# Optimization experiments

Measured on AMD Instinct MI355X. Metric: run time of the kernel, lower is better.

## Reference

```python
import jax, jax.numpy as jnp
import numpy as np

# loss weights / thresholds (match module defaults)
L_RC, L_HU, L_EDGE, L_TEX = 2.0, 1.5, 1.0, 0.8
L_HF, L_SYN, L_IC, L_MID, L_LF = 1.5, 1.0, 0.8, 0.8, 0.6
MIN_BODY, ART_FACTOR, FLAT_TH = 4096, 2.0, 0.03

SOBEL_X = jnp.array([[-1., 0., 1.], [-2., 0., 2.], [-1., 0., 1.]], jnp.float32)
SOBEL_Y = jnp.array([[-1., -2., -1.], [0., 0., 0.], [1., 2., 1.]], jnp.float32)
LAP = jnp.array([[0., 1., 0.], [1., -4., 1.], [0., 1., 0.]], jnp.float32)

def _conv2d(x, k):
    # x: (B,1,H,W), k: (kh,kw), 'same' padding single-channel conv
    kh, kw = k.shape
    return jax.lax.conv_general_dilated(
        x, k[None, None].astype(x.dtype), (1, 1),
        [(kh // 2, kh // 2), (kw // 2, kw // 2)],
        dimension_numbers=('NCHW', 'OIHW', 'NCHW'))

def _gauss_kernel(sigma):
    k = int(6 * sigma + 1)
    if k % 2 == 0:
        k += 1
    c = jnp.arange(k, dtype=jnp.float32) - k // 2
    g = jnp.exp(-0.5 * (c / sigma) ** 2)
    g = g / g.sum()
    return g[:, None] * g[None, :]

def _masked_mean(x, mask):
    cnt = jnp.sum(mask)
    return jnp.sum(jnp.where(mask, x, 0.0)) / jnp.maximum(cnt, 1)

def _masked_l1(a, b, mask):
    cnt = jnp.sum(mask)
    return jnp.sum(jnp.where(mask, jnp.abs(a - b), 0.0)) / jnp.maximum(cnt, 1)

def _masked_quantile(x, mask, q):
    # torch.quantile(x[mask], q) with linear interpolation
    v = jnp.sort(jnp.where(mask, x, jnp.inf).ravel())
    n = jnp.maximum(jnp.sum(mask), 1)
    pos = q * (n - 1).astype(x.dtype)
    lo = jnp.clip(jnp.floor(pos).astype(jnp.int32), 0, v.size - 1)
    hi = jnp.clip(jnp.ceil(pos).astype(jnp.int32), 0, v.size - 1)
    frac = pos - lo.astype(x.dtype)
    return v[lo] * (1.0 - frac) + v[hi] * frac

def setup_inputs() -> dict:
    key = jax.random.key(0)
    ks = jax.random.split(key, 7)
    B, H, W = 16, 768, 768
    return {
        'y_pred': jax.random.uniform(ks[0], (B, 1, 1, H, W), jnp.float32),
        'noise_pred': jax.random.normal(ks[1], (B, 1, 1, H, W), jnp.float32),
        'x_i': jax.random.uniform(ks[2], (B, 1, H, W), jnp.float32),
        'x_ip1': jax.random.uniform(ks[3], (B, 1, H, W), jnp.float32),
        'x_mid': jax.random.uniform(ks[4], (B, 1, H, W), jnp.float32),
        'W': jax.random.uniform(ks[5], (B, 1, H, W), jnp.float32),
        'noise_synthetic': jax.random.normal(ks[6], (B, 1, H, W), jnp.float32),
    }

def reference(y_pred, noise_pred, x_i, x_ip1, x_mid, W, noise_synthetic):
    yp = y_pred[:, :, 0]          # (B,1,H,W)
    npred = noise_pred[:, :, 0]

    # reconstruction
    loss_rc = jnp.mean(jnp.abs(yp * W - x_i * W))

    # HU consistency on body mask
    body = (x_i > 0.15) & (x_i < 0.85)
    nb = jnp.sum(body)
    mean_in = _masked_mean(x_i, body)
    mean_pr = _masked_mean(yp, body)
    hu = (mean_pr - mean_in) ** 2 + 0.5 * (
        (_masked_quantile(yp, body, 0.25) - _masked_quantile(x_i, body, 0.25)) ** 2
        + (_masked_quantile(yp, body, 0.75) - _masked_quantile(x_i, body, 0.75)) ** 2)
    loss_hu = jnp.where(nb > MIN_BODY, hu, 0.0)

    # edges
    gxp, gyp = _conv2d(yp, SOBEL_X), _conv2d(yp, SOBEL_Y)
    gxi, gyi = _conv2d(x_i, SOBEL_X), _conv2d(x_i, SOBEL_Y)
    loss_edge = jnp.mean(jnp.abs(gxp - gxi)) + jnp.mean(jnp.abs(gyp - gyi))

    gmi = jnp.sqrt(gxi ** 2 + gyi ** 2 + 1e-8)
    gmp = jnp.sqrt(gxp ** 2 + gyp ** 2 + 1e-8)

    # texture
    tex = (gmi > FLAT_TH) & (gmi < 0.5)
    loss_texture = jnp.where(jnp.sum(tex) > 100, _masked_l1(gmp, gmi, tex), 0.0)

    flat = gmi < FLAT_TH
    fb = flat & body
    nfb = jnp.sum(fb)

    # low/mid frequency losses on flat body regions
    G3, G1 = _gauss_kernel(3.0), _gauss_kernel(1.0)
    low_i, low_p, low_m = _conv2d(x_i, G3), _conv2d(yp, G3), _conv2d(x_mid, G3)
    lf = _masked_l1(low_p - low_m, 0.3 * (low_i - low_m), fb)
    mid_i = _conv2d(x_i, G1) - low_i
    mid_p = _conv2d(yp, G1) - low_p
    mid = _masked_l1(jnp.abs(mid_p), 0.3 * jnp.abs(mid_i), fb)
    loss_lf = jnp.where(nfb > 100, lf, 0.0)
    loss_mid = jnp.where(nfb > 100, mid, 0.0)

    # high-frequency noise via laplacian on flat regions
    lap_i, lap_p = _conv2d(x_i, LAP), _conv2d(yp, LAP)
    nf = jnp.sum(flat)
    loss_hf = jnp.where(nf > 100, _masked_l1(jnp.abs(lap_p), 0.3 * jnp.abs(lap_i), flat), 0.0)

    # synthetic noise supervision on flat body
    loss_syn = jnp.where(nfb > 100, _masked_l1(npred, noise_synthetic, fb), 0.0)

    # artifact penalty on flat regions
    ic = _masked_mean(jnp.maximum(gmp - ART_FACTOR * gmi, 0.0), flat)
    loss_ic = jnp.where(nf > 100, ic, 0.0)

    total = (L_RC * loss_rc + L_HU * loss_hu + L_EDGE * loss_edge
             + L_TEX * loss_texture + L_HF * loss_hf + L_MID * loss_mid
             + L_LF * loss_lf + L_SYN * loss_syn + L_IC * loss_ic)
    return total
```

## Files before the change

kernel.cpp:

```cpp
#include <hip/hip_runtime.h>


#define HH 768
#define WW 768
#define BB 16
#define HWSZ (HH * WW)
#define NPXD ((double)BB * (double)HWSZ)

#define NB 1024
#define NHIST (2 * NB)

#define STRIPS 3
#define HSEG 12
#define NSEG (HH / HSEG)
#define NJOBS (STRIPS * NSEG * BB)
#define NBLK1 (NJOBS / 4)

#define FBBUF 128

__device__ __forceinline__ float wredf(float v) {
#pragma unroll
  for (int o = 32; o > 0; o >>= 1) v += __shfl_down(v, o, 64);
  return v;
}
__device__ __forceinline__ unsigned wredu(unsigned v) {
#pragma unroll
  for (int o = 32; o > 0; o >>= 1) v += __shfl_down(v, o, 64);
  return v;
}

struct Row {
  float f[4];
  float l, r;
};

__device__ __forceinline__ Row load_row(const float* __restrict__ p, int y,
                                        int xl, int x0, int lane) {
  Row r;
  if (y < 0 || y >= HH) {
    r.f[0] = r.f[1] = r.f[2] = r.f[3] = 0.f;
    r.l = 0.f;
    r.r = 0.f;
    return r;
  }
  const float4 v = *(const float4*)(p + (size_t)y * WW + xl);
  r.f[0] = v.x; r.f[1] = v.y; r.f[2] = v.z; r.f[3] = v.w;
  float left = __shfl_up(v.w, 1, 64);
  float right = __shfl_down(v.x, 1, 64);
  if (lane == 0) left = (x0 > 0) ? p[(size_t)y * WW + x0 - 1] : 0.f;
  if (lane == 63) right = (x0 + 256 < WW) ? p[(size_t)y * WW + x0 + 256] : 0.f;
  r.l = left;
  r.r = right;
  return r;
}

#define LNB(row, j) ((j) == 0 ? (row).l : (row).f[(j)-1])
#define RNB(row, j) ((j) == 3 ? (row).r : (row).f[(j) + 1])


__global__ __launch_bounds__(256) void pass1_kernel(
    const float* __restrict__ yp, const float* __restrict__ xi,
    const float* __restrict__ wt, double* __restrict__ accs,
    unsigned* __restrict__ cnts, unsigned* __restrict__ fb_list, int fb_cap,
    unsigned* __restrict__ hist_final) {
  __shared__ unsigned s_hist[NHIST];
  __shared__ unsigned s_fb[4][FBBUF];
  __shared__ unsigned s_fbn[4];
  __shared__ float s_redf[4][8];
  __shared__ unsigned s_redc[4][3];

  const int tid = threadIdx.x;
  const int lane = tid & 63;
  const int wv = tid >> 6;
  const unsigned long long lmask_lt = (1ull << lane) - 1ull;

  for (int i = tid; i < NHIST; i += 256) s_hist[i] = 0u;
  if (lane == 0) s_fbn[wv] = 0u;
  __syncthreads();

  const int job = blockIdx.x * 4 + wv;
  const int s = job % STRIPS;
  const int seg = (job / STRIPS) % NSEG;
  const int b = job / (STRIPS * NSEG);
  const int x0 = s * 256;
  const int y0 = seg * HSEG;
  const int xl = x0 + lane * 4;
  const size_t base = (size_t)b * HWSZ;
  const float* ypb = yp + base;
  const float* xib = xi + base;
  const float* wtb = wt + base;

  float a_rc = 0.f, a_sxi = 0.f, a_syp = 0.f, a_ex = 0.f, a_ey = 0.f;
  float a_tex = 0.f, a_hf = 0.f, a_ic = 0.f;
  unsigned c_body = 0u, c_tex = 0u, c_flat = 0u;

  Row pm1 = load_row(ypb, y0 - 1, xl, x0, lane);
  Row pc = load_row(ypb, y0, xl, x0, lane);
  Row im1 = load_row(xib, y0 - 1, xl, x0, lane);
  Row icr = load_row(xib, y0, xl, x0, lane);

  for (int y = y0; y < y0 + HSEG; y++) {
    const Row pp1 = load_row(ypb, y + 1, xl, x0, lane);
    const Row ip1 = load_row(xib, y + 1, xl, x0, lane);
    const float4 w4 = *(const float4*)(wtb + (size_t)y * WW + xl);
    const float wf[4] = {w4.x, w4.y, w4.z, w4.w};

#pragma unroll
    for (int j = 0; j < 4; j++) {
      const float p00 = LNB(pm1, j), p01 = pm1.f[j], p02 = RNB(pm1, j);
      const float p10 = LNB(pc, j),  p11 = pc.f[j],  p12 = RNB(pc, j);
      const float p20 = LNB(pp1, j), p21 = pp1.f[j], p22 = RNB(pp1, j);
      const float i00 = LNB(im1, j), i01 = im1.f[j], i02 = RNB(im1, j);
      const float i10 = LNB(icr, j), i11 = icr.f[j], i12 = RNB(icr, j);
      const float i20 = LNB(ip1, j), i21 = ip1.f[j], i22 = RNB(ip1, j);

      const float gxp = (p02 - p00) + 2.f * (p12 - p10) + (p22 - p20);
      const float gyp = (p20 - p00) + 2.f * (p21 - p01) + (p22 - p02);
      const float lapp = p01 + p10 + p12 + p21 - 4.f * p11;
      const float gxi_ = (i02 - i00) + 2.f * (i12 - i10) + (i22 - i20);
      const float gyi_ = (i20 - i00) + 2.f * (i21 - i01) + (i22 - i02);
      const float lapi = i01 + i10 + i12 + i21 - 4.f * i11;

      const float yv = p11, xv = i11;
      a_rc += fabsf(yv * wf[j] - xv * wf[j]);

      const bool body = (xv > 0.15f) && (xv < 0.85f);
      if (body) {
        c_body++;
        a_sxi += xv;
        a_syp += yv;
        int bx = (int)(xv * (float)NB);
        bx = bx < 0 ? 0 : (bx > NB - 1 ? NB - 1 : bx);
        int by = (int)(yv * (float)NB);
        by = by < 0 ? 0 : (by > NB - 1 ? NB - 1 : by);
        atomicAdd(&s_hist[bx], 1u);
        atomicAdd(&s_hist[NB + by], 1u);
      }

      a_ex += fabsf(gxp - gxi_);
      a_ey += fabsf(gyp - gyi_);

      const float gmi = sqrtf(gxi_ * gxi_ + gyi_ * gyi_ + 1e-8f);
      const float gmp = sqrtf(gxp * gxp + gyp * gyp + 1e-8f);

      if (gmi > 0.03f && gmi < 0.5f) {
        c_tex++;
        a_tex += fabsf(gmp - gmi);
      }
      const bool flat = gmi < 0.03f;
      if (flat) {
        c_flat++;
        a_hf += fabsf(fabsf(lapp) - 0.3f * fabsf(lapi));
        a_ic += fmaxf(gmp - 2.0f * gmi, 0.f);
      }
      const bool qual = flat && body;
      const unsigned long long m = __ballot(qual);
      if (m) {
        const unsigned bofs = s_fbn[wv];
        if (qual) {
          const unsigned p = bofs + (unsigned)__popcll(m & lmask_lt);
          const unsigned gidx = (unsigned)(base + (size_t)y * WW + (xl + j));
          if (p < FBBUF) {
            s_fb[wv][p] = gidx;
          } else {
            const unsigned gi = atomicAdd(&cnts[3], 1u);
            if ((int)gi < fb_cap) fb_list[gi] = gidx;
          }
        }
        s_fbn[wv] = bofs + (unsigned)__popcll(m);
      }
    }
    pm1 = pc; pc = pp1;
    im1 = icr; icr = ip1;
  }

  {
    unsigned n = s_fbn[wv];
    if (n > FBBUF) n = FBBUF;
    unsigned gbase = 0u;
    if (lane == 0 && n > 0) gbase = atomicAdd(&cnts[3], n);
    gbase = __shfl(gbase, 0, 64);
    for (unsigned i = lane; i < n; i += 64) {
      const unsigned gi = gbase + i;
      if ((int)gi < fb_cap) fb_list[gi] = s_fb[wv][i];
    }
  }

  __syncthreads();
  for (int i = tid; i < NHIST; i += 256) {
    const unsigned v = s_hist[i];
    if (v) atomicAdd(&hist_final[i], v);
  }

  float f0 = wredf(a_rc), f1 = wredf(a_sxi), f2 = wredf(a_syp);
  float f3 = wredf(a_ex), f4 = wredf(a_ey), f5 = wredf(a_tex);
  float f6 = wredf(a_hf), f7 = wredf(a_ic);
  unsigned u0 = wredu(c_body), u1 = wredu(c_tex), u2 = wredu(c_flat);
  if (lane == 0) {
    s_redf[wv][0] = f0; s_redf[wv][1] = f1; s_redf[wv][2] = f2; s_redf[wv][3] = f3;
    s_redf[wv][4] = f4; s_redf[wv][5] = f5; s_redf[wv][6] = f6; s_redf[wv][7] = f7;
    s_redc[wv][0] = u0; s_redc[wv][1] = u1; s_redc[wv][2] = u2;
  }
  __syncthreads();
  if (tid < 8) {
    double sm = (double)s_redf[0][tid] + (double)s_redf[1][tid] +
                (double)s_redf[2][tid] + (double)s_redf[3][tid];
    atomicAdd(&accs[tid], sm);
  } else if (tid < 11) {
    int k = tid - 8;
    unsigned sm = s_redc[0][k] + s_redc[1][k] + s_redc[2][k] + s_redc[3][k];
    atomicAdd(&cnts[k], sm);
  }
}

__global__ __launch_bounds__(256) void pass2_kernel(
    const float* __restrict__ yp, const float* __restrict__ xi,
    const float* __restrict__ xm, const float* __restrict__ npred,
    const float* __restrict__ nsyn, double* __restrict__ accs,
    const unsigned* __restrict__ cnts, const unsigned* __restrict__ fb_list,
    int fb_cap) {
  __shared__ float w3[19];
  __shared__ float w1[7];
  __shared__ double s_red[4][3];
  const int tid = threadIdx.x;
  const int lane = tid & 63;
  const int wv = tid >> 6;

  if (tid == 0) {
    float tmp[19], s = 0.f;
    for (int i = 0; i < 19; i++) {
      float c = (float)(i - 9) / 3.0f;
      tmp[i] = expf(-0.5f * c * c);
      s += tmp[i];
    }
    for (int i = 0; i < 19; i++) w3[i] = tmp[i] / s;
    float tmp1[7], s1 = 0.f;
    for (int i = 0; i < 7; i++) {
      float c = (float)(i - 3);
      tmp1[i] = expf(-0.5f * c * c);
      s1 += tmp1[i];
    }
    for (int i = 0; i < 7; i++) w1[i] = tmp1[i] / s1;
  }
  __syncthreads();

  unsigned nfb = cnts[3];
  if (nfb > (unsigned)fb_cap) nfb = (unsigned)fb_cap;
  const int wid = (int)((blockIdx.x * blockDim.x + tid) >> 6);
  const int nwaves = (int)((gridDim.x * blockDim.x) >> 6);

  double w_lf = 0.0, w_md = 0.0, w_sy = 0.0;

  for (int i = wid; i < (int)nfb; i += nwaves) {
    const unsigned px = fb_list[i];
    const int b = (int)(px / (unsigned)HWSZ);
    const int rem = (int)(px % (unsigned)HWSZ);
    const int y = rem / WW;
    const int x = rem % WW;
    const size_t base = (size_t)b * HWSZ;
    const float* xib = xi + base;
    const float* ypb = yp + base;
    const float* xmb = xm + base;

    float npv = 0.f, nsv = 0.f;
    if (lane == 0) { npv = npred[px]; nsv = nsyn[px]; }

    float s_li = 0.f, s_lp = 0.f, s_lm = 0.f;
    float s_gi = 0.f, s_gp = 0.f;
    const bool interior = (y >= 9) && (y < HH - 9) && (x >= 9) && (x < WW - 9);
    if (interior) {
#pragma unroll
      for (int k = 0; k < 6; k++) {
        const int tap = lane + 64 * k;
        if (tap < 361) {
          const int r = tap / 19, c = tap - r * 19;
          const float wgt = w3[r] * w3[c];
          const int o = (y + r - 9) * WW + (x + c - 9);
          s_li += wgt * xib[o];
          s_lp += wgt * ypb[o];
          s_lm += wgt * xmb[o];
        }
      }
      if (lane < 49) {
        const int r = lane / 7, c = lane - r * 7;
        const float wgt = w1[r] * w1[c];
        const int o = (y + r - 3) * WW + (x + c - 3);
        s_gi = wgt * xib[o];
        s_gp = wgt * ypb[o];
      }
    } else {
#pragma unroll
      for (int k = 0; k < 6; k++) {
        const int tap = lane + 64 * k;
        if (tap < 361) {
          const int r = tap / 19, c = tap - r * 19;
          const int gy = y + r - 9, gx = x + c - 9;
          if (gy >= 0 && gy < HH && gx >= 0 && gx < WW) {
            const float wgt = w3[r] * w3[c];
            const int o = gy * WW + gx;
            s_li += wgt * xib[o];
            s_lp += wgt * ypb[o];
            s_lm += wgt * xmb[o];
          }
        }
      }
      if (lane < 49) {
        const int r = lane / 7, c = lane - r * 7;
        const int gy = y + r - 3, gx = x + c - 3;
        if (gy >= 0 && gy < HH && gx >= 0 && gx < WW) {
          const float wgt = w1[r] * w1[c];
          const int o = gy * WW + gx;
          s_gi = wgt * xib[o];
          s_gp = wgt * ypb[o];
        }
      }
    }
    s_li = wredf(s_li);
    s_lp = wredf(s_lp);
    s_lm = wredf(s_lm);
    s_gi = wredf(s_gi);
    s_gp = wredf(s_gp);
    if (lane == 0) {
      const float lf = fabsf((s_lp - s_lm) - 0.3f * (s_li - s_lm));
      const float mi_ = s_gi - s_li, mp_ = s_gp - s_lp;
      const float md = fabsf(fabsf(mp_) - 0.3f * fabsf(mi_));
      w_lf += (double)lf;
      w_md += (double)md;
      w_sy += (double)fabsf(npv - nsv);
    }
  }

  if (lane == 0) {
    s_red[wv][0] = w_lf; s_red[wv][1] = w_md; s_red[wv][2] = w_sy;
  }
  __syncthreads();
  if (tid < 3) {
    const double t = s_red[0][tid] + s_red[1][tid] + s_red[2][tid] + s_red[3][tid];
    if (t != 0.0) atomicAdd(&accs[8 + tid], t);
  }
}

__global__ __launch_bounds__(256) void finalize_kernel(
    const double* __restrict__ accs, const unsigned* __restrict__ cnts,
    const unsigned* __restrict__ hist, float* __restrict__ out) {
  __shared__ unsigned sc[NHIST];
  __shared__ unsigned wsum[8];
  __shared__ double quant[4];
  const int tid = threadIdx.x;
  const int lane = tid & 63;
  const int wv = tid >> 6;

  if (tid < 4) quant[tid] = 0.0;

#pragma unroll
  for (int h = 0; h < 2; h++) {
    const int baseh = h * NB + tid * 4;
    const unsigned v0 = hist[baseh + 0];
    const unsigned v1 = hist[baseh + 1];
    const unsigned v2 = hist[baseh + 2];
    const unsigned v3 = hist[baseh + 3];
    const unsigned s = v0 + v1 + v2 + v3;
    unsigned scl = s;
#pragma unroll
    for (int o = 1; o < 64; o <<= 1) {
      const unsigned t = __shfl_up(scl, o, 64);
      if (lane >= o) scl += t;
    }
    if (lane == 63) wsum[h * 4 + wv] = scl;
    __syncthreads();
    unsigned woff = 0;
    for (int k = 0; k < wv; k++) woff += wsum[h * 4 + k];
    const unsigned excl = woff + scl - s;
    const unsigned c0 = excl + v0;
    const unsigned c1 = c0 + v1;
    const unsigned c2 = c1 + v2;
    const unsigned c3 = c2 + v3;
    sc[baseh + 0] = c0;
    sc[baseh + 1] = c1;
    sc[baseh + 2] = c2;
    sc[baseh + 3] = c3;
    __syncthreads();
  }

  const unsigned nb = cnts[0];
  if (tid < 4 && nb > 4096u) {
    const int h = tid >> 1;
    const double q = (tid & 1) ? 0.75 : 0.25;
    const double pos = q * (double)(nb - 1u);
    int lo = 0, hi = NB - 1;
    while (lo < hi) {
      const int mid = (lo + hi) >> 1;
      if ((double)sc[h * NB + mid] > pos) hi = mid; else lo = mid + 1;
    }
    const unsigned cum_before = (lo > 0) ? sc[h * NB + lo - 1] : 0u;
    const unsigned m = sc[h * NB + lo] - cum_before;
    const double local = pos - (double)cum_before;
    quant[tid] = ((double)lo + (local + 0.5) / (double)(m ? m : 1u)) *
                 (1.0 / (double)NB);
  }
  __syncthreads();
  if (tid != 0) return;

  const unsigned ntex = cnts[1], nflat = cnts[2], nfb = cnts[3];
  const double loss_rc = accs[0] / NPXD;
  const double denb = (double)(nb > 0u ? nb : 1u);
  const double mean_in = accs[1] / denb;
  const double mean_pr = accs[2] / denb;

  double loss_hu = 0.0;
  if (nb > 4096u) {
    const double q25i = quant[0], q75i = quant[1];
    const double q25p = quant[2], q75p = quant[3];
    const double d = mean_pr - mean_in;
    loss_hu = d * d + 0.5 * ((q25p - q25i) * (q25p - q25i) +
                             (q75p - q75i) * (q75p - q75i));
  }

  const double loss_edge = accs[3] / NPXD + accs[4] / NPXD;
  const double loss_tex = (ntex > 100u) ? accs[5] / (double)(ntex ? ntex : 1u) : 0.0;
  const double loss_hf = (nflat > 100u) ? accs[6] / (double)(nflat ? nflat : 1u) : 0.0;
  const double loss_ic = (nflat > 100u) ? accs[7] / (double)(nflat ? nflat : 1u) : 0.0;
  const double denfb = (double)(nfb > 0u ? nfb : 1u);
  const double loss_lf = (nfb > 100u) ? accs[8] / denfb : 0.0;
  const double loss_mid = (nfb > 100u) ? accs[9] / denfb : 0.0;
  const double loss_syn = (nfb > 100u) ? accs[10] / denfb : 0.0;

  const double total = 2.0 * loss_rc + 1.5 * loss_hu + 1.0 * loss_edge +
                       0.8 * loss_tex + 1.5 * loss_hf + 0.8 * loss_mid +
                       0.6 * loss_lf + 1.0 * loss_syn + 0.8 * loss_ic;
  out[0] = (float)total;
}

extern "C" void kernel_launch(void* const* d_in, const int* in_sizes, int n_in,
                              void* d_out, int out_size, void* d_ws,
                              size_t ws_size, hipStream_t stream) {
  (void)in_sizes; (void)n_in; (void)out_size;
  const float* y_pred = (const float*)d_in[0];
  const float* noise_pred = (const float*)d_in[1];
  const float* x_i = (const float*)d_in[2];
  const float* x_mid = (const float*)d_in[4];
  const float* Wt = (const float*)d_in[5];
  const float* nsyn = (const float*)d_in[6];
  float* out = (float*)d_out;

  char* ws = (char*)d_ws;
  double* accs = (double*)ws;
  unsigned* cnts = (unsigned*)(ws + 128);
  unsigned* hist_final = (unsigned*)(ws + 256);
  const size_t FIXED = 16384;

  size_t avail = (ws_size > FIXED) ? (ws_size - FIXED) : 0;
  long long cap = (long long)(avail / 4);
  if (cap > (long long)BB * HWSZ) cap = (long long)BB * HWSZ;
  int fb_cap = (int)cap;
  unsigned* fb_list = (unsigned*)(ws + FIXED);

  hipMemsetAsync(ws, 0, FIXED, stream);
  pass1_kernel<<<NBLK1, 256, 0, stream>>>(y_pred, x_i, Wt, accs, cnts,
                                          fb_list, fb_cap, hist_final);
  pass2_kernel<<<256, 256, 0, stream>>>(y_pred, x_i, x_mid, noise_pred, nsyn,
                                        accs, cnts, fb_list, fb_cap);
  finalize_kernel<<<1, 256, 0, stream>>>(accs, cnts, hist_final, out);
}
```

Before: 262.1 us.

## Prefetch rows in pass1, shrink segments, stage histograms per block, widen pass2

Pass1 now prefetches the next row of y_pred, x_i and W one iteration ahead, halves the row-segment height to launch twice as many blocks, and sets a minimum-occupancy launch bound. Per-block shared histograms are written to a partials buffer and summed by a new reduction kernel, replacing global atomics. Pass2 grid doubles and the flat-body list capacity is capped at 4 MB. The extra launch, the partials traffic, and the halo rows reloaded by the shorter segments add cost, and a too-small fb_cap could drop entries from the list.

New measurement: 461.8 us. +76.2%, slower.

```diff
diff --git a/kernel.cpp b/kernel.cpp
--- a/kernel.cpp
+++ b/kernel.cpp
@@ -11,7 +11,7 @@
 #define NHIST (2 * NB)
 
 #define STRIPS 3
-#define HSEG 12
+#define HSEG 6
 #define NSEG (HH / HSEG)
 #define NJOBS (STRIPS * NSEG * BB)
 #define NBLK1 (NJOBS / 4)
@@ -54,15 +54,23 @@
   return r;
 }
 
+__device__ __forceinline__ Row zero_row() {
+  Row r;
+  r.f[0] = r.f[1] = r.f[2] = r.f[3] = 0.f;
+  r.l = 0.f; r.r = 0.f;
+  return r;
+}
+
 #define LNB(row, j) ((j) == 0 ? (row).l : (row).f[(j)-1])
 #define RNB(row, j) ((j) == 3 ? (row).r : (row).f[(j) + 1])
 
 
-__global__ __launch_bounds__(256) void pass1_kernel(
+__global__ __launch_bounds__(256, 5) void pass1_kernel(
     const float* __restrict__ yp, const float* __restrict__ xi,
     const float* __restrict__ wt, double* __restrict__ accs,
     unsigned* __restrict__ cnts, unsigned* __restrict__ fb_list, int fb_cap,
-    unsigned* __restrict__ hist_final) {
+    unsigned* __restrict__ hist_final, unsigned* __restrict__ hist_parts,
+    int use_parts) {
   __shared__ unsigned s_hist[NHIST];
   __shared__ unsigned s_fb[4][FBBUF];
   __shared__ unsigned s_fbn[4];
@@ -95,14 +103,25 @@
   unsigned c_body = 0u, c_tex = 0u, c_flat = 0u;
 
   Row pm1 = load_row(ypb, y0 - 1, xl, x0, lane);
-  Row pc = load_row(ypb, y0, xl, x0, lane);
+  Row pc  = load_row(ypb, y0,     xl, x0, lane);
+  Row pp1 = load_row(ypb, y0 + 1, xl, x0, lane);
   Row im1 = load_row(xib, y0 - 1, xl, x0, lane);
-  Row icr = load_row(xib, y0, xl, x0, lane);
+  Row icr = load_row(xib, y0,     xl, x0, lane);
+  Row ip1 = load_row(xib, y0 + 1, xl, x0, lane);
+  float4 w4 = *(const float4*)(wtb + (size_t)y0 * WW + xl);
 
   for (int y = y0; y < y0 + HSEG; y++) {
-    const Row pp1 = load_row(ypb, y + 1, xl, x0, lane);
-    const Row ip1 = load_row(xib, y + 1, xl, x0, lane);
-    const float4 w4 = *(const float4*)(wtb + (size_t)y * WW + xl);
+    Row pn, inx;
+    float4 w4n = make_float4(0.f, 0.f, 0.f, 0.f);
+    if (y + 2 <= y0 + HSEG) {
+      pn  = load_row(ypb, y + 2, xl, x0, lane);
+      inx = load_row(xib, y + 2, xl, x0, lane);
+    } else {
+      pn = zero_row(); inx = zero_row();
+    }
+    if (y + 1 < y0 + HSEG)
+      w4n = *(const float4*)(wtb + (size_t)(y + 1) * WW + xl);
+
     const float wf[4] = {w4.x, w4.y, w4.z, w4.w};
 
 #pragma unroll
@@ -170,8 +189,9 @@
         s_fbn[wv] = bofs + (unsigned)__popcll(m);
       }
     }
-    pm1 = pc; pc = pp1;
-    im1 = icr; icr = ip1;
+    pm1 = pc; pc = pp1; pp1 = pn;
+    im1 = icr; icr = ip1; ip1 = inx;
+    w4 = w4n;
   }
 
   {
@@ -187,9 +207,14 @@
   }
 
   __syncthreads();
-  for (int i = tid; i < NHIST; i += 256) {
-    const unsigned v = s_hist[i];
-    if (v) atomicAdd(&hist_final[i], v);
+  if (use_parts) {
+    unsigned* row = hist_parts + (size_t)blockIdx.x * NHIST;
+    for (int i = tid; i < NHIST; i += 256) row[i] = s_hist[i];
+  } else {
+    for (int i = tid; i < NHIST; i += 256) {
+      const unsigned v = s_hist[i];
+      if (v) atomicAdd(&hist_final[i], v);
+    }
   }
 
   float f0 = wredf(a_rc), f1 = wredf(a_sxi), f2 = wredf(a_syp);
@@ -211,6 +236,22 @@
     unsigned sm = s_redc[0][k] + s_redc[1][k] + s_redc[2][k] + s_redc[3][k];
     atomicAdd(&cnts[k], sm);
   }
+}
+
+__global__ __launch_bounds__(256) void hist_reduce_kernel(
+    const unsigned* __restrict__ hist_parts, unsigned* __restrict__ hist_final,
+    int nparts) {
+  unsigned acc[8];
+#pragma unroll
+  for (int k = 0; k < 8; k++) acc[k] = 0u;
+  for (int p = blockIdx.x; p < nparts; p += gridDim.x) {
+    const unsigned* row = hist_parts + (size_t)p * NHIST;
+#pragma unroll
+    for (int k = 0; k < 8; k++) acc[k] += row[threadIdx.x + k * 256];
+  }
+#pragma unroll
+  for (int k = 0; k < 8; k++)
+    if (acc[k]) atomicAdd(&hist_final[threadIdx.x + k * 256], acc[k]);
 }
 
 __global__ __launch_bounds__(256) void pass2_kernel(
@@ -449,16 +490,32 @@
   unsigned* hist_final = (unsigned*)(ws + 256);
   const size_t FIXED = 16384;
 
-  size_t avail = (ws_size > FIXED) ? (ws_size - FIXED) : 0;
-  long long cap = (long long)(avail / 4);
-  if (cap > (long long)BB * HWSZ) cap = (long long)BB * HWSZ;
-  int fb_cap = (int)cap;
+  const size_t avail = (ws_size > FIXED) ? (ws_size - FIXED) : 0;
+  const size_t parts_bytes = (size_t)NBLK1 * NHIST * 4;
+  int use_parts = 0;
+  int fb_cap = 0;
   unsigned* fb_list = (unsigned*)(ws + FIXED);
+  unsigned* hist_parts = (unsigned*)(ws + FIXED);
+
+  if (avail >= parts_bytes + (1u << 20)) {
+    use_parts = 1;
+    size_t fb_bytes = avail - parts_bytes;
+    if (fb_bytes > (1u << 22)) fb_bytes = (1u << 22);
+    fb_cap = (int)(fb_bytes / 4);
+    hist_parts = (unsigned*)(ws + FIXED + fb_bytes);
+  } else {
+    size_t fb_bytes = avail;
+    if (fb_bytes > (1u << 22)) fb_bytes = (1u << 22);
+    fb_cap = (int)(fb_bytes / 4);
+  }
 
   hipMemsetAsync(ws, 0, FIXED, stream);
   pass1_kernel<<<NBLK1, 256, 0, stream>>>(y_pred, x_i, Wt, accs, cnts,
-                                          fb_list, fb_cap, hist_final);
-  pass2_kernel<<<256, 256, 0, stream>>>(y_pred, x_i, x_mid, noise_pred, nsyn,
+                                          fb_list, fb_cap, hist_final,
+                                          hist_parts, use_parts);
+  if (use_parts)
+    hist_reduce_kernel<<<64, 256, 0, stream>>>(hist_parts, hist_final, NBLK1);
+  pass2_kernel<<<512, 256, 0, stream>>>(y_pred, x_i, x_mid, noise_pred, nsyn,
                                         accs, cnts, fb_list, fb_cap);
   finalize_kernel<<<1, 256, 0, stream>>>(accs, cnts, hist_final, out);
 }
```
